# Performance work log

Hardware: AMD Instinct MI355X
Metric: run time of the kernel (lower is better)

The kernel has to match this reference:

```python
import jax, jax.numpy as jnp
import numpy as np

NUM_HOPS = 2
GAMMA = 0.8


def setup_inputs() -> dict:
    key = jax.random.key(0)
    ks = jax.random.split(key, 17)
    B, L, V, E, M, Mt, R = 8, 128, 50257, 768, 400, 800, 40
    W = 0.02  # init scale for learned params
    return {
        'hidden_states': jax.random.normal(ks[0], (B, L, E), jnp.float32),
        'wte': jax.random.normal(ks[1], (V, E), jnp.float32) * W,
        'rel_emb': jax.random.normal(ks[2], (R, E), jnp.float32) * W,
        'W_s': jax.random.normal(ks[3], (NUM_HOPS, E, E), jnp.float32) * W,
        'W_n': jax.random.normal(ks[4], (NUM_HOPS, E, E), jnp.float32) * W,
        'W_r': jax.random.normal(ks[5], (NUM_HOPS, E, E), jnp.float32) * W,
        'W_triple': jax.random.normal(ks[6], (E, 3 * E), jnp.float32) * W,
        'gate_w': jax.random.normal(ks[7], (E,), jnp.float32) * W,
        'gate_b': jnp.zeros((), jnp.float32),
        'concept_ids': jax.random.randint(ks[8], (B, M), 0, V),
        'relation_ids': jax.random.randint(ks[9], (B, Mt), 0, R),
        'head_idx': jax.random.randint(ks[10], (B, Mt), 0, M),
        'tail_idx': jax.random.randint(ks[11], (B, Mt), 0, M),
        'triple_labels': jax.random.randint(ks[12], (B, Mt), 0, 2),
        'distances': jax.random.randint(ks[13], (B, M), 0, 3),
        'vocab_map': jax.random.randint(ks[14], (V,), 0, M),
        'map_mask': jax.random.randint(ks[15], (V,), 0, 2),
    }


def _triple_encoder(wte, rel_emb, W_s, W_n, W_r, concept_ids, relation_ids, head_idx, tail_idx):
    concept_repr = wte[concept_ids]      # B,M,E
    rel_repr = rel_emb[relation_ids]     # B,Mt,E

    def gcn(cr, rr, h, t):               # per-batch CompGCN, faithful to torch loop
        M = cr.shape[0]
        ch, rh = cr, rr
        for l in range(NUM_HOPS):
            upd = jnp.zeros_like(cr)
            upd = upd.at[t].add(cr[h] - rr)   # scatter_add(o) + scatter_add(-rel)
            upd = upd.at[h].add(cr[t] - rr)
            cnt = jnp.zeros((M,), cr.dtype).at[t].add(1.0).at[h].add(1.0)
            upd = cr @ W_s[l].T + (upd @ W_n[l].T) / jnp.clip(cnt, 1.0, None)[:, None]
            ch = jax.nn.relu(upd)
            rh = rr @ W_r[l].T
        return ch, rh

    node, relh = jax.vmap(gcn)(concept_repr, rel_repr, head_idx, tail_idx)
    E = node.shape[-1]
    hi = jnp.broadcast_to(head_idx[:, :, None], head_idx.shape + (E,))
    ti = jnp.broadcast_to(tail_idx[:, :, None], tail_idx.shape + (E,))
    hrep = jnp.take_along_axis(node, hi, axis=1)
    trep = jnp.take_along_axis(node, ti, axis=1)
    return jnp.concatenate([hrep, relh, trep], axis=-1)  # B,Mt,3E


def _multi_hop(triple_prob, distances, head, tail):
    B, L, Mt = triple_prob.shape
    M = distances.shape[1]
    dt = triple_prob.dtype
    init_mask = jnp.broadcast_to((distances == 0).astype(dt)[:, None, :], (B, L, M))
    decay = (0.8 ** distances.astype(dt))[:, None, :]
    head_b = jnp.broadcast_to(head[:, None, :], (B, L, Mt))

    def scatter_mean(vals, t):  # vals: L,Mt  t: Mt -> L,M
        s = jnp.zeros((L, M), vals.dtype).at[:, t].add(vals)
        c = jnp.zeros((M,), vals.dtype).at[t].add(1.0)
        return s / jnp.clip(c, 1.0, None)

    node_score = init_mask
    total = init_mask * (-100000.0)
    for _ in range(NUM_HOPS):
        ths = jnp.take_along_axis(node_score, head_b, axis=2)  # B,L,Mt
        upd = ths * GAMMA + triple_prob
        node_score = jax.vmap(scatter_mean)(upd, tail)          # B,L,M
        total = total + node_score * decay
    return total


def reference(hidden_states, wte, rel_emb, W_s, W_n, W_r, W_triple, gate_w, gate_b,
              concept_ids, relation_ids, head_idx, tail_idx, triple_labels,
              distances, vocab_map, map_mask):
    triple_repr = _triple_encoder(wte, rel_emb, W_s, W_n, W_r,
                                  concept_ids, relation_ids, head_idx, tail_idx)
    lm_probs = jax.nn.softmax(hidden_states @ wte.T, axis=-1)            # B,L,V
    tl = triple_repr @ W_triple.T                                        # B,Mt,E
    triple_prob = jax.nn.sigmoid(jnp.einsum('ble,bme->blm', hidden_states, tl))
    triple_prob = triple_prob * (triple_labels != -1)[:, None, :].astype(triple_prob.dtype)
    scores = _multi_hop(triple_prob, distances, head_idx, tail_idx)      # B,L,M
    concept_probs = jax.nn.softmax(scores, axis=-1)
    cpv = concept_probs[:, :, vocab_map]                                 # gather into vocab: B,L,V
    cpv = cpv * (map_mask != 0)[None, None, :].astype(cpv.dtype)
    gate = jax.nn.sigmoid(hidden_states @ gate_w + gate_b)[..., None]    # B,L,1
    probs = gate * cpv + (1.0 - gate) * lm_probs
    return probs
```

## Files before the change

### kernel.cpp

```cpp
#include <hip/hip_runtime.h>
#include <stdint.h>

#define HB 8
#define HL 128
#define HV 50257
#define HE 768
#define HM 400
#define HMT 800
#define HBL (HB*HL)
#define NTILES 393
#define ELD 50272

typedef __attribute__((ext_vector_type(4))) float f32x4;
typedef __attribute__((ext_vector_type(8))) short bf16x8;
typedef unsigned short u16;

struct u16x4 { u16 x, y, z, w; };

__device__ __forceinline__ u16 f2bf(float x){
  union { float f; uint32_t u; } v; v.f = x;
  uint32_t r = v.u + 0x7fffu + ((v.u >> 16) & 1u);
  return (u16)(r >> 16);
}
__device__ __forceinline__ float bf2f(u16 b){
  union { uint32_t u; float f; } v; v.u = ((uint32_t)b) << 16;
  return v.f;
}
__device__ __forceinline__ void glds(const u16* g, const u16* l){
  __builtin_amdgcn_global_load_lds(
      (const __attribute__((address_space(1))) void*)g,
      (__attribute__((address_space(3))) void*)l, 16, 0, 0);
}

__global__ __launch_bounds__(256) void cvt4_k(const float* __restrict__ src,
                                              u16* __restrict__ dst, long n4){
  long i = (long)blockIdx.x * 256 + threadIdx.x;
  long stride = (long)gridDim.x * 256;
  for (; i < n4; i += stride) {
    const float4 x = ((const float4*)src)[i];
    u16x4 y; y.x = f2bf(x.x); y.y = f2bf(x.y); y.z = f2bf(x.z); y.w = f2bf(x.w);
    ((u16x4*)dst)[i] = y;
  }
}

__global__ __launch_bounds__(256) void prep_k(const float* __restrict__ hs,
    const float* __restrict__ rel, const float* __restrict__ Wr1src,
    const float* __restrict__ Wtsrc, const float* __restrict__ Ws1,
    const float* __restrict__ Wn1, const int* __restrict__ vmap,
    const int* __restrict__ mmask, u16* __restrict__ hid_b, u16* __restrict__ rel_b,
    u16* __restrict__ wr1, u16* __restrict__ wt_b, u16* __restrict__ wcat,
    int* __restrict__ vmm){
  const int b = blockIdx.x, t = threadIdx.x;
  if (b < 768) {
    int i = b*256 + t;
    float4 x = ((const float4*)hs)[i];
    u16x4 y; y.x=f2bf(x.x); y.y=f2bf(x.y); y.z=f2bf(x.z); y.w=f2bf(x.w);
    ((u16x4*)hid_b)[i] = y;
  } else if (b < 798) {
    int i = (b-768)*256 + t;
    float4 x = ((const float4*)rel)[i];
    u16x4 y; y.x=f2bf(x.x); y.y=f2bf(x.y); y.z=f2bf(x.z); y.w=f2bf(x.w);
    ((u16x4*)rel_b)[i] = y;
  } else if (b < 1374) {
    int i = (b-798)*256 + t;
    float4 x = ((const float4*)Wr1src)[i];
    u16x4 y; y.x=f2bf(x.x); y.y=f2bf(x.y); y.z=f2bf(x.z); y.w=f2bf(x.w);
    ((u16x4*)wr1)[i] = y;
  } else if (b < 3102) {
    int i = (b-1374)*256 + t;
    float4 x = ((const float4*)Wtsrc)[i];
    u16x4 y; y.x=f2bf(x.x); y.y=f2bf(x.y); y.z=f2bf(x.z); y.w=f2bf(x.w);
    ((u16x4*)wt_b)[i] = y;
  } else if (b < 5406) {
    int i = (b-3102)*256 + t;
    int e = i / HE, k = i - e*HE;
    wcat[(long)e*(2*HE) + k]      = f2bf(Ws1[i]);
    wcat[(long)e*(2*HE) + HE + k] = f2bf(Wn1[i]);
  } else {
    int base = (b-5406)*1024 + t*4;
    #pragma unroll
    for (int i = 0; i < 4; ++i) {
      int c = base + i;
      if (c < HV) vmm[c] = mmask[c] ? vmap[c] : -1;
    }
  }
}

__global__ __launch_bounds__(256) void gcn_scatter_k(const float* __restrict__ wte,
    const float* __restrict__ rel, const int* __restrict__ cids,
    const int* __restrict__ rids, const int* __restrict__ head,
    const int* __restrict__ tail, u16* __restrict__ An){
  const int ch = blockIdx.x % 48;
  const int b  = blockIdx.x / 48;
  const int e0 = ch * 16;
  __shared__ float cw[HM][17];
  __shared__ float upd[HM][17];
  __shared__ float relc[40][17];
  __shared__ float cnt[HM];
  const int tid = threadIdx.x;

  for (int idx = tid; idx < HM*16; idx += 256) {
    int m = idx >> 4, e = idx & 15;
    cw[m][e] = wte[(long)cids[b*HM+m]*HE + e0 + e];
    upd[m][e] = 0.f;
  }
  for (int idx = tid; idx < 40*16; idx += 256) {
    int r = idx >> 4, e = idx & 15;
    relc[r][e] = rel[r*HE + e0 + e];
  }
  for (int m = tid; m < HM; m += 256) cnt[m] = 0.f;
  __syncthreads();

  for (int j = tid; j < HMT; j += 256) {
    int h = head[b*HMT+j], t = tail[b*HMT+j], r = rids[b*HMT+j];
    atomicAdd(&cnt[t], 1.f);
    atomicAdd(&cnt[h], 1.f);
    #pragma unroll
    for (int e = 0; e < 16; ++e) {
      float rv = relc[r][e];
      atomicAdd(&upd[t][e], cw[h][e] - rv);
      atomicAdd(&upd[h][e], cw[t][e] - rv);
    }
  }
  __syncthreads();

  for (int idx = tid; idx < HM*16; idx += 256) {
    int m = idx >> 4, e = idx & 15;
    float ic = 1.f / fmaxf(cnt[m], 1.f);
    u16* dst = An + ((long)b*HM + m) * (2*HE);
    dst[e0 + e]      = f2bf(cw[m][e]);
    dst[HE + e0 + e] = f2bf(upd[m][e] * ic);
  }
}

template<int ACT, int OUTBF16, int BIG, int DUALB>
__global__ __launch_bounds__(256) void gemm_bt(
    const u16* __restrict__ A, const u16* __restrict__ Bm,
    const u16* __restrict__ Bm2, void* __restrict__ Cout,
    float* __restrict__ rowpart,
    int Mdim, int Ndim, int Kdim, int lda, int ldb, int ldc,
    long Abs, long Bbs, long Cbs, long Coff2)
{
  __shared__ alignas(16) u16 Asm[128*64];
  __shared__ alignas(16) u16 Bsm[128*64];
  int mtile, ntile, bz;
  if (BIG) {
    const int wg = (blockIdx.x & 7) * NTILES + (blockIdx.x >> 3);
    mtile = wg & 7; ntile = wg >> 3; bz = 0;
  } else {
    mtile = blockIdx.x; ntile = blockIdx.y; bz = blockIdx.z;
  }
  const int zb = DUALB ? (bz & 7) : bz;
  const bool alt = DUALB && (bz >= 8);
  const u16* Ab = A + (long)zb * Abs;
  const u16* Bb = (alt ? Bm2 : Bm) + (long)zb * Bbs;
  const int m0 = mtile * 128;
  const int n0 = ntile * 128;
  const int tid = threadIdx.x;
  const int lane = tid & 63;
  const int wid = tid >> 6;
  const int wr = wid >> 1, wc = wid & 1;
  const int srw = lane >> 3;
  const int sl  = lane & 7;

  f32x4 acc[4][4] = {};

  for (int k0 = 0; k0 < Kdim; k0 += 64) {
    #pragma unroll
    for (int i = 0; i < 4; ++i) {
      const int c = i*4 + wid;
      const int row = c*8 + srw;
      const int koff = k0 + ((sl ^ srw) * 8);
      int ra = m0 + row; if (ra > Mdim-1) ra = Mdim-1;
      glds(Ab + (long)ra * lda + koff, &Asm[c*512]);
      int rn = n0 + row; if (rn > Ndim-1) rn = Ndim-1;
      glds(Bb + (long)rn * ldb + koff, &Bsm[c*512]);
    }
    __syncthreads();
    #pragma unroll
    for (int kk = 0; kk < 2; ++kk) {
      bf16x8 af[4], bfr[4];
      #pragma unroll
      for (int mi = 0; mi < 4; ++mi) {
        const int R = wr*64 + mi*16 + (lane & 15);
        af[mi] = *(const bf16x8*)&Asm[R*64 + (((kk*4 + (lane>>4)) ^ (R & 7)) * 8)];
      }
      #pragma unroll
      for (int ni = 0; ni < 4; ++ni) {
        const int R = wc*64 + ni*16 + (lane & 15);
        bfr[ni] = *(const bf16x8*)&Bsm[R*64 + (((kk*4 + (lane>>4)) ^ (R & 7)) * 8)];
      }
      #pragma unroll
      for (int mi = 0; mi < 4; ++mi)
        #pragma unroll
        for (int ni = 0; ni < 4; ++ni)
          acc[mi][ni] = __builtin_amdgcn_mfma_f32_16x16x32_bf16(af[mi], bfr[ni], acc[mi][ni], 0, 0, 0);
    }
    __syncthreads();
  }

  const int cr0 = m0 + wr*64 + ((lane >> 4) * 4);
  const int cc0 = n0 + wc*64 + (lane & 15);

  if (BIG) {
    float* rs = (float*)Asm;
    #pragma unroll
    for (int mi = 0; mi < 4; ++mi) {
      #pragma unroll
      for (int r = 0; r < 4; ++r) {
        const int rowi = cr0 + mi*16 + r;
        float s = 0.f;
        #pragma unroll
        for (int ni = 0; ni < 4; ++ni) {
          const int col = cc0 + ni*16;
          if (col < Ndim) {
            float e = __expf(acc[mi][ni][r]);
            if (OUTBF16) ((u16*)Cout)[(long)rowi*ELD + col] = f2bf(e);
            else        ((float*)Cout)[(long)rowi*HV + col] = e;
            s += e;
          }
        }
        s += __shfl_xor(s, 8); s += __shfl_xor(s, 4);
        s += __shfl_xor(s, 2); s += __shfl_xor(s, 1);
        if ((lane & 15) == 0)
          rs[wc*128 + wr*64 + mi*16 + ((lane >> 4) << 2) + r] = s;
      }
    }
    __syncthreads();
    if (tid < 128)
      rowpart[(long)(m0 + tid) * NTILES + ntile] = rs[tid] + rs[128 + tid];
    return;
  }

  const long cb = (long)zb * Cbs + (alt ? Coff2 : 0);
  #pragma unroll
  for (int mi = 0; mi < 4; ++mi) {
    #pragma unroll
    for (int ni = 0; ni < 4; ++ni) {
      const int col = cc0 + ni*16;
      if (col < Ndim) {
        #pragma unroll
        for (int r = 0; r < 4; ++r) {
          const int rowi = cr0 + mi*16 + r;
          if (rowi < Mdim) {
            float v = acc[mi][ni][r];
            if (ACT == 1) v = fmaxf(v, 0.f);
            if (OUTBF16) ((u16*)Cout)[cb + (long)rowi*ldc + col] = f2bf(v);
            else        ((float*)Cout)[cb + (long)rowi*ldc + col] = v;
          }
        }
      }
    }
  }
}

__global__ __launch_bounds__(256) void multihop_k(const float* __restrict__ scores,
    const float* __restrict__ hs, const float* __restrict__ gw,
    const float* __restrict__ gb,
    const int* __restrict__ head, const int* __restrict__ tail,
    const int* __restrict__ rids, const int* __restrict__ labels,
    const int* __restrict__ dist, float* __restrict__ gatev,
    float* __restrict__ cprob){
  const int bl = blockIdx.x;
  const int b = bl >> 7;
  const int tid = threadIdx.x;
  const int lane = tid & 63, wid = tid >> 6;
  __shared__ float srow[840];
  __shared__ float tp[HMT];
  __shared__ float ns[HM], sacc[HM], tot[HM], invc[HM], dec[HM];
  __shared__ float red[16];
  __shared__ float gred[4];
  const int* hb = head + b*HMT;
  const int* tb = tail + b*HMT;
  const int* rb = rids + b*HMT;
  const int* lb = labels + b*HMT;
  const float* sr = scores + (long)bl * 840;

  float gs = 0.f;
  for (int e = tid; e < HE; e += 256) gs += hs[(long)bl*HE + e] * gw[e];
  for (int o = 32; o; o >>= 1) gs += __shfl_down(gs, o);
  if (lane == 0) gred[wid] = gs;

  for (int i = tid; i < 840; i += 256) srow[i] = sr[i];
  for (int m = tid; m < HM; m += 256) {
    int d = dist[b*HM + m];
    float im = (d == 0) ? 1.f : 0.f;
    ns[m] = im; tot[m] = im * -100000.f;
    dec[m] = (d == 0) ? 1.f : ((d == 1) ? 0.8f : 0.64f);
    sacc[m] = 0.f; invc[m] = 0.f;
  }
  __syncthreads();
  if (tid == 0)
    gatev[bl] = 1.f / (1.f + __expf(-(gred[0]+gred[1]+gred[2]+gred[3] + gb[0])));
  for (int j = tid; j < HMT; j += 256) {
    atomicAdd(&invc[tb[j]], 1.f);
    float x = srow[hb[j]] + srow[400 + tb[j]] + srow[800 + rb[j]];
    tp[j] = (lb[j] == -1) ? 0.f : 1.f / (1.f + __expf(-x));
  }
  __syncthreads();
  for (int m = tid; m < HM; m += 256) invc[m] = 1.f / fmaxf(invc[m], 1.f);
  __syncthreads();

  for (int hop = 0; hop < 2; ++hop) {
    for (int j = tid; j < HMT; j += 256) {
      float u = ns[hb[j]] * 0.8f + tp[j];
      atomicAdd(&sacc[tb[j]], u);
    }
    __syncthreads();
    for (int m = tid; m < HM; m += 256) {
      float v = sacc[m] * invc[m];
      ns[m] = v; tot[m] += v * dec[m]; sacc[m] = 0.f;
    }
    __syncthreads();
  }

  float lmx = -3.4e38f;
  for (int m = tid; m < HM; m += 256) lmx = fmaxf(lmx, tot[m]);
  for (int o = 32; o; o >>= 1) lmx = fmaxf(lmx, __shfl_down(lmx, o));
  if (lane == 0) red[wid] = lmx;
  __syncthreads();
  float gmx = fmaxf(fmaxf(red[0], red[1]), fmaxf(red[2], red[3]));
  float ls = 0.f;
  for (int m = tid; m < HM; m += 256) ls += __expf(tot[m] - gmx);
  for (int o = 32; o; o >>= 1) ls += __shfl_down(ls, o);
  if (lane == 0) red[8 + wid] = ls;
  __syncthreads();
  float inv = 1.f / (red[8] + red[9] + red[10] + red[11]);
  float* outrow = cprob + (long)bl * HM;
  for (int m = tid; m < HM; m += 256) outrow[m] = __expf(tot[m] - gmx) * inv;
}

template<int EXPBF>
__global__ __launch_bounds__(256) void finalize_k(const void* __restrict__ expl,
    const float* __restrict__ rowpart, const float* __restrict__ gatev,
    const float* __restrict__ cprob, const int* __restrict__ vmm,
    float* __restrict__ out){
  const int r = blockIdx.x / 13;
  const int ch = blockIdx.x - r*13;
  const int tid = threadIdx.x;
  __shared__ float red[4];
  __shared__ float cpl[HM];
  float s = 0.f;
  for (int t = tid; t < NTILES; t += 256) s += rowpart[r*NTILES + t];
  for (int o = 32; o; o >>= 1) s += __shfl_down(s, o);
  if ((tid & 63) == 0) red[tid >> 6] = s;
  const float g = gatev[r];
  for (int m = tid; m < HM; m += 256) cpl[m] = g * cprob[r*HM + m];
  __syncthreads();
  const float scale = (1.f - g) / (red[0] + red[1] + red[2] + red[3]);
  const u16* erb = (const u16*)expl + (long)r * ELD;
  const float* erf = (const float*)expl + (long)r * HV;
  float* orow = out + (long)r * HV;
  #pragma unroll
  for (int it = 0; it < 2; ++it) {
    const int c = ch*4096 + it*2048 + tid*8;
    if (c + 8 <= HV) {
      float e[8];
      if (EXPBF) {
        bf16x8 v = *(const bf16x8*)&erb[c];
        #pragma unroll
        for (int i = 0; i < 8; ++i) e[i] = bf2f((u16)v[i]);
      } else {
        float4 a = *(const float4*)&erf[c];
        float4 b2 = *(const float4*)&erf[c+4];
        e[0]=a.x; e[1]=a.y; e[2]=a.z; e[3]=a.w;
        e[4]=b2.x; e[5]=b2.y; e[6]=b2.z; e[7]=b2.w;
      }
      int4 v0 = *(const int4*)&vmm[c];
      int4 v1 = *(const int4*)&vmm[c+4];
      const int ix[8] = {v0.x, v0.y, v0.z, v0.w, v1.x, v1.y, v1.z, v1.w};
      float o8[8];
      #pragma unroll
      for (int i = 0; i < 8; ++i)
        o8[i] = (ix[i] >= 0 ? cpl[ix[i]] : 0.f) + scale * e[i];
      *(float4*)&orow[c]   = make_float4(o8[0], o8[1], o8[2], o8[3]);
      *(float4*)&orow[c+4] = make_float4(o8[4], o8[5], o8[6], o8[7]);
    } else if (c < HV) {
      for (int i = 0; i < 8 && c + i < HV; ++i) {
        float e = EXPBF ? bf2f(((const u16*)expl)[(long)r*ELD + c + i]) : erf[c+i];
        int ix = vmm[c+i];
        orow[c+i] = (ix >= 0 ? cpl[ix] : 0.f) + scale * e;
      }
    }
  }
}

extern "C" void kernel_launch(void* const* d_in, const int* in_sizes, int n_in,
                              void* d_out, int out_size, void* d_ws, size_t ws_size,
                              hipStream_t stream)
{
  const float* hs   = (const float*)d_in[0];
  const float* wte  = (const float*)d_in[1];
  const float* rel  = (const float*)d_in[2];
  const float* Ws   = (const float*)d_in[3];
  const float* Wn   = (const float*)d_in[4];
  const float* Wr   = (const float*)d_in[5];
  const float* Wt   = (const float*)d_in[6];
  const float* gw   = (const float*)d_in[7];
  const float* gb   = (const float*)d_in[8];
  const int* cids   = (const int*)d_in[9];
  const int* rids   = (const int*)d_in[10];
  const int* head   = (const int*)d_in[11];
  const int* tail   = (const int*)d_in[12];
  const int* labels = (const int*)d_in[13];
  const int* dist   = (const int*)d_in[14];
  const int* vmap   = (const int*)d_in[15];
  const int* mmask  = (const int*)d_in[16];
  float* out = (float*)d_out;

  char* ws = (char*)d_ws;
  size_t o = 0;
  auto alloc = [&](size_t bytes) -> char* {
    char* p = ws + o; o = (o + bytes + 255) & ~(size_t)255; return p;
  };
  u16* wte_b     = (u16*)alloc((size_t)HV*HE*2);
  u16* hid_b     = (u16*)alloc((size_t)HBL*HE*2);
  float* cprob   = (float*)alloc((size_t)HBL*HM*4);
  float* rowpart = (float*)alloc((size_t)HBL*NTILES*4);
  float* gatev   = (float*)alloc(HBL*4);
  int* vmm       = (int*)alloc((size_t)HV*4);

  const bool bigws = ws_size >= (size_t)196*1024*1024;
  u16* expl = (u16*)(ws + o);
  u16* wcat  = (u16*)alloc((size_t)HE*2*HE*2);
  u16* wr1   = (u16*)alloc((size_t)HE*HE*2);
  u16* wt_b  = (u16*)alloc((size_t)HE*3*HE*2);
  u16* rel_b = (u16*)alloc((size_t)40*HE*2);
  u16* anode = (u16*)alloc((size_t)HB*HM*2*HE*2);
  u16* nodeb = (u16*)alloc((size_t)HB*HM*HE*2);
  u16* relWr = (u16*)alloc((size_t)40*HE*2);
  float* scores = (float*)alloc((size_t)HB*HL*840*4);
  u16* P13   = (u16*)alloc((size_t)HB*840*HE*2);
  (void)in_sizes; (void)n_in; (void)out_size;

  prep_k<<<5456, 256, 0, stream>>>(hs, rel, Wr + (size_t)HE*HE, Wt,
      Ws + (size_t)HE*HE, Wn + (size_t)HE*HE, vmap, mmask,
      hid_b, rel_b, wr1, wt_b, wcat, vmm);

  gcn_scatter_k<<<HB*48, 256, 0, stream>>>(wte, rel, cids, rids, head, tail, anode);

  gemm_bt<1,1,0,0><<<dim3(4,6,8), 256, 0, stream>>>(anode, wcat, nullptr, nodeb,
      nullptr, HM, HE, 2*HE, 2*HE, 2*HE, HE, (long)HM*2*HE, 0, (long)HM*HE, 0);
  gemm_bt<0,1,0,0><<<dim3(1,6,1), 256, 0, stream>>>(rel_b, wr1, nullptr, relWr,
      nullptr, 40, HE, HE, HE, HE, HE, 0, 0, 0, 0);
  gemm_bt<0,1,0,0><<<dim3(1,6,8), 256, 0, stream>>>(relWr, wt_b + HE, nullptr,
      P13 + (long)800*HE, nullptr,
      40, HE, HE, HE, 3*HE, HE, 0, 0, (long)840*HE, 0);
  gemm_bt<0,1,0,1><<<dim3(4,6,16), 256, 0, stream>>>(nodeb, wt_b, wt_b + 2*HE,
      P13, nullptr,
      HM, HE, HE, HE, 3*HE, HE, (long)HM*HE, 0, (long)840*HE, (long)HM*HE);
  gemm_bt<0,0,0,0><<<dim3(1,7,8), 256, 0, stream>>>(hid_b, P13, nullptr, scores,
      nullptr, HL, 840, HE, HE, HE, 840, (long)HL*HE, (long)840*HE, (long)HL*840, 0);

  multihop_k<<<HBL, 256, 0, stream>>>(scores, hs, gw, gb, head, tail, rids,
      labels, dist, gatev, cprob);

  cvt4_k<<<4096, 256, 0, stream>>>(wte, wte_b, (long)HV*HE/4);

  if (bigws) {
    gemm_bt<0,1,1,0><<<3144, 256, 0, stream>>>(hid_b, wte_b, nullptr, expl,
        rowpart, HBL, HV, HE, HE, HE, ELD, 0, 0, 0, 0);
    finalize_k<1><<<HBL*13, 256, 0, stream>>>(expl, rowpart, gatev, cprob,
        vmm, out);
  } else {
    gemm_bt<0,0,1,0><<<3144, 256, 0, stream>>>(hid_b, wte_b, nullptr, out,
        rowpart, HBL, HV, HE, HE, HE, HV, 0, 0, 0, 0);
    finalize_k<0><<<HBL*13, 256, 0, stream>>>(out, rowpart, gatev, cprob,
        vmm, out);
  }
}
```

Before: 461.6 us.

## Double-buffer GEMM LDS tiles, merge small GEMMs, fold wte conversion into prep

```diff
diff --git a/kernel.cpp b/kernel.cpp
--- a/kernel.cpp
+++ b/kernel.cpp
@@ -32,25 +32,24 @@
       (__attribute__((address_space(3))) void*)l, 16, 0, 0);
 }
 
-__global__ __launch_bounds__(256) void cvt4_k(const float* __restrict__ src,
-                                              u16* __restrict__ dst, long n4){
-  long i = (long)blockIdx.x * 256 + threadIdx.x;
-  long stride = (long)gridDim.x * 256;
-  for (; i < n4; i += stride) {
-    const float4 x = ((const float4*)src)[i];
-    u16x4 y; y.x = f2bf(x.x); y.y = f2bf(x.y); y.z = f2bf(x.z); y.w = f2bf(x.w);
-    ((u16x4*)dst)[i] = y;
-  }
-}
-
 __global__ __launch_bounds__(256) void prep_k(const float* __restrict__ hs,
     const float* __restrict__ rel, const float* __restrict__ Wr1src,
     const float* __restrict__ Wtsrc, const float* __restrict__ Ws1,
     const float* __restrict__ Wn1, const int* __restrict__ vmap,
-    const int* __restrict__ mmask, u16* __restrict__ hid_b, u16* __restrict__ rel_b,
+    const int* __restrict__ mmask, const float* __restrict__ wte,
+    u16* __restrict__ hid_b, u16* __restrict__ rel_b,
     u16* __restrict__ wr1, u16* __restrict__ wt_b, u16* __restrict__ wcat,
-    int* __restrict__ vmm){
+    int* __restrict__ vmm, u16* __restrict__ wte_b){
   const int b = blockIdx.x, t = threadIdx.x;
+  if (b >= 5456) {
+    long i = (long)(b-5456)*256 + t;
+    if (i < (long)HV*HE/4) {
+      float4 x = ((const float4*)wte)[i];
+      u16x4 y; y.x=f2bf(x.x); y.y=f2bf(x.y); y.z=f2bf(x.z); y.w=f2bf(x.w);
+      ((u16x4*)wte_b)[i] = y;
+    }
+    return;
+  }
   if (b < 768) {
     int i = b*256 + t;
     float4 x = ((const float4*)hs)[i];
@@ -133,27 +132,13 @@
   }
 }
 
-template<int ACT, int OUTBF16, int BIG, int DUALB>
-__global__ __launch_bounds__(256) void gemm_bt(
-    const u16* __restrict__ A, const u16* __restrict__ Bm,
-    const u16* __restrict__ Bm2, void* __restrict__ Cout,
-    float* __restrict__ rowpart,
+template<int ACT, int OUTBF16, int BIG>
+__device__ __forceinline__ void gemm_core(
+    const u16* __restrict__ Ab, const u16* __restrict__ Bb,
+    void* __restrict__ Cout, float* __restrict__ rowpart,
     int Mdim, int Ndim, int Kdim, int lda, int ldb, int ldc,
-    long Abs, long Bbs, long Cbs, long Coff2)
+    int mtile, int ntile, u16* AsmB, u16* BsmB)
 {
-  __shared__ alignas(16) u16 Asm[128*64];
-  __shared__ alignas(16) u16 Bsm[128*64];
-  int mtile, ntile, bz;
-  if (BIG) {
-    const int wg = (blockIdx.x & 7) * NTILES + (blockIdx.x >> 3);
-    mtile = wg & 7; ntile = wg >> 3; bz = 0;
-  } else {
-    mtile = blockIdx.x; ntile = blockIdx.y; bz = blockIdx.z;
-  }
-  const int zb = DUALB ? (bz & 7) : bz;
-  const bool alt = DUALB && (bz >= 8);
-  const u16* Ab = A + (long)zb * Abs;
-  const u16* Bb = (alt ? Bm2 : Bm) + (long)zb * Bbs;
   const int m0 = mtile * 128;
   const int n0 = ntile * 128;
   const int tid = threadIdx.x;
@@ -165,30 +150,41 @@
 
   f32x4 acc[4][4] = {};
 
-  for (int k0 = 0; k0 < Kdim; k0 += 64) {
+  auto stage = [&](int buf, int k0) {
+    u16* As = AsmB + buf*8192;
+    u16* Bs = BsmB + buf*8192;
     #pragma unroll
     for (int i = 0; i < 4; ++i) {
       const int c = i*4 + wid;
       const int row = c*8 + srw;
       const int koff = k0 + ((sl ^ srw) * 8);
       int ra = m0 + row; if (ra > Mdim-1) ra = Mdim-1;
-      glds(Ab + (long)ra * lda + koff, &Asm[c*512]);
+      glds(Ab + (long)ra * lda + koff, &As[c*512]);
       int rn = n0 + row; if (rn > Ndim-1) rn = Ndim-1;
-      glds(Bb + (long)rn * ldb + koff, &Bsm[c*512]);
-    }
-    __syncthreads();
+      glds(Bb + (long)rn * ldb + koff, &Bs[c*512]);
+    }
+  };
+
+  const int NT = Kdim >> 6;
+  stage(0, 0);
+  __syncthreads();
+  int cur = 0;
+  for (int t = 0; t < NT; ++t) {
+    if (t + 1 < NT) stage(cur ^ 1, (t + 1) << 6);
+    const u16* As = AsmB + cur*8192;
+    const u16* Bs = BsmB + cur*8192;
     #pragma unroll
     for (int kk = 0; kk < 2; ++kk) {
       bf16x8 af[4], bfr[4];
       #pragma unroll
       for (int mi = 0; mi < 4; ++mi) {
         const int R = wr*64 + mi*16 + (lane & 15);
-        af[mi] = *(const bf16x8*)&Asm[R*64 + (((kk*4 + (lane>>4)) ^ (R & 7)) * 8)];
+        af[mi] = *(const bf16x8*)&As[R*64 + (((kk*4 + (lane>>4)) ^ (R & 7)) * 8)];
       }
       #pragma unroll
       for (int ni = 0; ni < 4; ++ni) {
         const int R = wc*64 + ni*16 + (lane & 15);
-        bfr[ni] = *(const bf16x8*)&Bsm[R*64 + (((kk*4 + (lane>>4)) ^ (R & 7)) * 8)];
+        bfr[ni] = *(const bf16x8*)&Bs[R*64 + (((kk*4 + (lane>>4)) ^ (R & 7)) * 8)];
       }
       #pragma unroll
       for (int mi = 0; mi < 4; ++mi)
@@ -197,13 +193,14 @@
           acc[mi][ni] = __builtin_amdgcn_mfma_f32_16x16x32_bf16(af[mi], bfr[ni], acc[mi][ni], 0, 0, 0);
     }
     __syncthreads();
+    cur ^= 1;
   }
 
   const int cr0 = m0 + wr*64 + ((lane >> 4) * 4);
   const int cc0 = n0 + wc*64 + (lane & 15);
 
   if (BIG) {
-    float* rs = (float*)Asm;
+    float* rs = (float*)AsmB;
     #pragma unroll
     for (int mi = 0; mi < 4; ++mi) {
       #pragma unroll
@@ -232,7 +229,6 @@
     return;
   }
 
-  const long cb = (long)zb * Cbs + (alt ? Coff2 : 0);
   #pragma unroll
   for (int mi = 0; mi < 4; ++mi) {
     #pragma unroll
@@ -245,11 +241,71 @@
           if (rowi < Mdim) {
             float v = acc[mi][ni][r];
             if (ACT == 1) v = fmaxf(v, 0.f);
-            if (OUTBF16) ((u16*)Cout)[cb + (long)rowi*ldc + col] = f2bf(v);
-            else        ((float*)Cout)[cb + (long)rowi*ldc + col] = v;
+            if (OUTBF16) ((u16*)Cout)[(long)rowi*ldc + col] = f2bf(v);
+            else        ((float*)Cout)[(long)rowi*ldc + col] = v;
           }
         }
       }
+    }
+  }
+}
+
+template<int ACT, int OUTBF16, int BIG>
+__global__ __launch_bounds__(256) void gemm_bt(
+    const u16* __restrict__ A, const u16* __restrict__ Bm,
+    void* __restrict__ Cout, float* __restrict__ rowpart,
+    int Mdim, int Ndim, int Kdim, int lda, int ldb, int ldc,
+    long Abs, long Bbs, long Cbs)
+{
+  __shared__ alignas(16) u16 Asm[2*8192];
+  __shared__ alignas(16) u16 Bsm[2*8192];
+  int mtile, ntile, bz;
+  if (BIG) {
+    const int wg = (blockIdx.x & 7) * NTILES + (blockIdx.x >> 3);
+    mtile = wg & 7; ntile = wg >> 3; bz = 0;
+  } else {
+    mtile = blockIdx.x; ntile = blockIdx.y; bz = blockIdx.z;
+  }
+  const u16* Ab = A + (long)bz * Abs;
+  const u16* Bb = Bm + (long)bz * Bbs;
+  void* Cb = OUTBF16 ? (void*)((u16*)Cout + (long)bz * Cbs)
+                     : (void*)((float*)Cout + (long)bz * Cbs);
+  gemm_core<ACT,OUTBF16,BIG>(Ab, Bb, Cb, rowpart, Mdim, Ndim, Kdim,
+                             lda, ldb, ldc, mtile, ntile, Asm, Bsm);
+}
+
+template<int PHASE>
+__global__ __launch_bounds__(256) void gemm_multi(
+    const u16* __restrict__ anode, const u16* __restrict__ wcat,
+    u16* __restrict__ nodeb, const u16* __restrict__ rel_b,
+    const u16* __restrict__ wr1, u16* __restrict__ relWr,
+    const u16* __restrict__ wt_b, u16* __restrict__ P13)
+{
+  __shared__ alignas(16) u16 Asm[2*8192];
+  __shared__ alignas(16) u16 Bsm[2*8192];
+  const int mtile = blockIdx.x, ntile = blockIdx.y, z = blockIdx.z;
+  if (PHASE == 0) {
+    if (z < 8) {
+      gemm_core<1,1,0>(anode + (long)z*HM*2*HE, wcat, nodeb + (long)z*HM*HE,
+          nullptr, HM, HE, 2*HE, 2*HE, 2*HE, HE, mtile, ntile, Asm, Bsm);
+    } else {
+      if (mtile) return;
+      gemm_core<0,1,0>(rel_b, wr1, relWr, nullptr,
+          40, HE, HE, HE, HE, HE, 0, ntile, Asm, Bsm);
+    }
+  } else {
+    if (z < 8) {
+      if (mtile) return;
+      gemm_core<0,1,0>(relWr, wt_b + HE, P13 + (long)z*840*HE + (long)800*HE,
+          nullptr, 40, HE, HE, HE, 3*HE, HE, 0, ntile, Asm, Bsm);
+    } else if (z < 16) {
+      gemm_core<0,1,0>(nodeb + (long)(z-8)*HM*HE, wt_b,
+          P13 + (long)(z-8)*840*HE, nullptr,
+          HM, HE, HE, HE, 3*HE, HE, mtile, ntile, Asm, Bsm);
+    } else {
+      gemm_core<0,1,0>(nodeb + (long)(z-16)*HM*HE, wt_b + 2*HE,
+          P13 + (long)(z-16)*840*HE + (long)HM*HE, nullptr,
+          HM, HE, HE, HE, 3*HE, HE, mtile, ntile, Asm, Bsm);
     }
   }
 }
@@ -433,38 +489,30 @@
   u16* P13   = (u16*)alloc((size_t)HB*840*HE*2);
   (void)in_sizes; (void)n_in; (void)out_size;
 
-  prep_k<<<5456, 256, 0, stream>>>(hs, rel, Wr + (size_t)HE*HE, Wt,
-      Ws + (size_t)HE*HE, Wn + (size_t)HE*HE, vmap, mmask,
-      hid_b, rel_b, wr1, wt_b, wcat, vmm);
+  prep_k<<<5456 + 37693, 256, 0, stream>>>(hs, rel, Wr + (size_t)HE*HE, Wt,
+      Ws + (size_t)HE*HE, Wn + (size_t)HE*HE, vmap, mmask, wte,
+      hid_b, rel_b, wr1, wt_b, wcat, vmm, wte_b);
 
   gcn_scatter_k<<<HB*48, 256, 0, stream>>>(wte, rel, cids, rids, head, tail, anode);
 
-  gemm_bt<1,1,0,0><<<dim3(4,6,8), 256, 0, stream>>>(anode, wcat, nullptr, nodeb,
-      nullptr, HM, HE, 2*HE, 2*HE, 2*HE, HE, (long)HM*2*HE, 0, (long)HM*HE, 0);
-  gemm_bt<0,1,0,0><<<dim3(1,6,1), 256, 0, stream>>>(rel_b, wr1, nullptr, relWr,
-      nullptr, 40, HE, HE, HE, HE, HE, 0, 0, 0, 0);
-  gemm_bt<0,1,0,0><<<dim3(1,6,8), 256, 0, stream>>>(relWr, wt_b + HE, nullptr,
-      P13 + (long)800*HE, nullptr,
-      40, HE, HE, HE, 3*HE, HE, 0, 0, (long)840*HE, 0);
-  gemm_bt<0,1,0,1><<<dim3(4,6,16), 256, 0, stream>>>(nodeb, wt_b, wt_b + 2*HE,
-      P13, nullptr,
-      HM, HE, HE, HE, 3*HE, HE, (long)HM*HE, 0, (long)840*HE, (long)HM*HE);
-  gemm_bt<0,0,0,0><<<dim3(1,7,8), 256, 0, stream>>>(hid_b, P13, nullptr, scores,
-      nullptr, HL, 840, HE, HE, HE, 840, (long)HL*HE, (long)840*HE, (long)HL*840, 0);
+  gemm_multi<0><<<dim3(4,6,9), 256, 0, stream>>>(anode, wcat, nodeb,
+      rel_b, wr1, relWr, wt_b, P13);
+  gemm_multi<1><<<dim3(4,6,24), 256, 0, stream>>>(anode, wcat, nodeb,
+      rel_b, wr1, relWr, wt_b, P13);
+  gemm_bt<0,0,0><<<dim3(1,7,8), 256, 0, stream>>>(hid_b, P13, scores,
+      nullptr, HL, 840, HE, HE, HE, 840, (long)HL*HE, (long)840*HE, (long)HL*840);
 
   multihop_k<<<HBL, 256, 0, stream>>>(scores, hs, gw, gb, head, tail, rids,
       labels, dist, gatev, cprob);
 
-  cvt4_k<<<4096, 256, 0, stream>>>(wte, wte_b, (long)HV*HE/4);
-
   if (bigws) {
-    gemm_bt<0,1,1,0><<<3144, 256, 0, stream>>>(hid_b, wte_b, nullptr, expl,
-        rowpart, HBL, HV, HE, HE, HE, ELD, 0, 0, 0, 0);
+    gemm_bt<0,1,1><<<3144, 256, 0, stream>>>(hid_b, wte_b, expl, rowpart,
+        HBL, HV, HE, HE, HE, ELD, 0, 0, 0);
     finalize_k<1><<<HBL*13, 256, 0, stream>>>(expl, rowpart, gatev, cprob,
         vmm, out);
   } else {
-    gemm_bt<0,0,1,0><<<3144, 256, 0, stream>>>(hid_b, wte_b, nullptr, out,
-        rowpart, HBL, HV, HE, HE, HE, HV, 0, 0, 0, 0);
+    gemm_bt<0,0,1><<<3144, 256, 0, stream>>>(hid_b, wte_b, out, rowpart,
+        HBL, HV, HE, HE, HE, HV, 0, 0, 0);
     finalize_k<0><<<HBL*13, 256, 0, stream>>>(out, rowpart, gatev, cprob,
         vmm, out);
   }
```

Result: slower. 488.0 us (+5.7%).
